# Performance work log

Measured on AMD Instinct MI355X. Metric: run time of the kernel, lower is better.

The kernel has to match this reference:

```python
import jax, jax.numpy as jnp
import numpy as np

B, N, NODE, EDIM, LAT, ENC = 4, 512, 3, 1, 32, 32
NEG = -jnp.inf


def _xavier(key, fan_in, fan_out):
    a = jnp.sqrt(6.0 / (fan_in + fan_out))
    return jax.random.uniform(key, (fan_in, fan_out), jnp.float32, -a, a)


def _mpnn(z, enc_e, adj_b, Wm, Wu):
    """Message: linear([z_i, z_j, e_ij]); adjacency-masked max-aggregation; update linear."""
    zd = z.shape[-1]
    zi = jnp.broadcast_to(z[:, :, None, :], (B, N, N, zd))
    zj = jnp.broadcast_to(z[:, None, :, :], (B, N, N, zd))
    msg = jnp.concatenate([zi, zj, enc_e], axis=-1) @ Wm          # [B,N,N,LAT]
    msg = jnp.where(adj_b[..., None], msg, NEG)
    agg = jnp.max(msg, axis=2)                                    # max over neighbors j
    return jnp.concatenate([z, agg], axis=-1) @ Wu                # [B,N,LAT]


def setup_inputs() -> dict:
    key = jax.random.key(0)
    ks = jax.random.split(key, 16)
    x = jax.random.normal(ks[0], (B, N, NODE), jnp.float32)
    h = jax.random.normal(ks[1], (B, N, LAT), jnp.float32)
    adj = jax.random.randint(ks[2], (B, N, N), 0, 2, jnp.int32)
    e_feat = jax.random.uniform(ks[3], (B, N, N, EDIM), jnp.float32)
    Wn = _xavier(ks[4], LAT + NODE, ENC)          # node_encoder
    We = _xavier(ks[5], EDIM, ENC)                # edge_encoder
    Wm = _xavier(ks[6], 2 * ENC + ENC, LAT)       # processor message
    Wu = _xavier(ks[7], ENC + LAT, LAT)           # processor update
    Wtm = _xavier(ks[8], 2 * LAT + ENC, LAT)      # termination_mpnn message
    Wtu = _xavier(ks[9], LAT + LAT, LAT)          # termination_mpnn update
    Wd = _xavier(ks[10], LAT + ENC, NODE)         # decoder
    Wt = _xavier(ks[11], LAT, 1)                  # termination head
    Wp = _xavier(ks[12], 2 * LAT + ENC, 1)        # predecessor head (pred=1)
    return {"x": x, "h": h, "adj": adj, "e_feat": e_feat, "Wn": Wn, "We": We,
            "Wm": Wm, "Wu": Wu, "Wtm": Wtm, "Wtu": Wtu, "Wd": Wd, "Wt": Wt, "Wp": Wp}


def reference(x, h, adj, e_feat, Wn, We, Wm, Wu, Wtm, Wtu, Wd, Wt, Wp):
    adj2 = adj + jnp.eye(N, dtype=adj.dtype)[None]                # add self-loops
    adj_b = adj2.astype(bool)
    z = jnp.concatenate([x, h], axis=-1) @ Wn                     # [B,N,ENC]
    enc_e = e_feat @ We                                           # [B,N,N,ENC]
    new_h = _mpnn(z, enc_e, adj_b, Wm, Wu) + z                    # [B,N,LAT]
    new_x = jnp.concatenate([z, new_h], axis=-1) @ Wd             # [B,N,NODE]
    tau_node = _mpnn(new_h, enc_e, adj_b, Wtm, Wtu)               # [B,N,LAT]
    tau = jnp.mean(tau_node, axis=1) @ Wt                         # [B,1]
    # predecessor head: all-pairs [h_i, h_j, e_ij] -> scalar, masked by adjacency
    hi = jnp.broadcast_to(new_h[:, :, None, :], (B, N, N, LAT))
    hj = jnp.broadcast_to(new_h[:, None, :, :], (B, N, N, LAT))
    p = (jnp.concatenate([hi, hj, enc_e], axis=-1) @ Wp)[..., 0]  # [B,N,N]
    p = jnp.where(adj_b, p, NEG)
    return new_x, p, tau, new_h
```

## Files before the change

### kernel.cpp

```cpp
#include <hip/hip_runtime.h>

#define XN 512
#define XB 4
#define XSENT (-1.0e30f)
#define XNEG (-3.402823466e38f)

__device__ __forceinline__ float xscrub(float v) {
    unsigned u = __float_as_uint(v);
    u = ((u & 0x7f800000u) == 0x7f800000u) ? 0xff7fffffu : u;
    return __uint_as_float(u);
}

__global__ __launch_bounds__(64) void ne2y_g0(
    const float* __restrict__ We, const float* __restrict__ Wm,
    const float* __restrict__ Wtm, const float* __restrict__ Wtu,
    const float* __restrict__ Wt, const float* __restrict__ Wp,
    float* __restrict__ drv, float* __restrict__ tau_out)
{
    const int t = threadIdx.x;
    if (t < 32) {
        float c1 = 0.f, c2 = 0.f;
        for (int k = 0; k < 32; ++k) {
            const float w = We[k];
            c1 += w * Wm[(64 + k) * 32 + t];
            c2 += w * Wtm[(64 + k) * 32 + t];
        }
        drv[t]      = c1;
        drv[32 + t] = c2;
        float u1 = 0.f, u2 = 0.f;
        for (int k = 0; k < 32; ++k) {
            u1 += Wtu[t * 32 + k]        * Wt[k];
            u2 += Wtu[(32 + t) * 32 + k] * Wt[k];
        }
        drv[64 + t] = u1;
        drv[96 + t] = u2;
        if (t == 0) {
            float cp = 0.f;
            for (int k = 0; k < 32; ++k) cp += We[k] * Wp[64 + k];
            drv[128] = cp;
        }
    }
    if (t < XB) tau_out[t] = 0.f;
}

__global__ __launch_bounds__(256) void ne2y_g1(
    const float* __restrict__ x, const float* __restrict__ h,
    const float* __restrict__ Wn, const float* __restrict__ Wm,
    float* __restrict__ z, float* __restrict__ A1, float* __restrict__ B1)
{
    const int t = threadIdx.x;
    const int r = t >> 5;
    const int l = t & 31;
    const int row = blockIdx.x * 8 + r;
    float acc = 0.f;
    {
        const float* xr = x + row * 3;
        const float* hr = h + row * 32;
        for (int k = 0; k < 3; ++k)  acc += xr[k] * Wn[k * 32 + l];
        for (int k = 0; k < 32; ++k) acc += hr[k] * Wn[(3 + k) * 32 + l];
    }
    __shared__ float zs[8][32];
    zs[r][l] = acc;
    z[row * 32 + l] = acc;
    __syncthreads();
    float a = 0.f, bb = 0.f;
    for (int k = 0; k < 32; ++k) {
        const float zk = zs[r][k];
        a  += zk * Wm[k * 32 + l];
        bb += zk * Wm[(32 + k) * 32 + l];
    }
    A1[row * 32 + l] = a;
    B1[row * 32 + l] = bb;
}

__global__ __launch_bounds__(256) void ne2y_m2(
    const int* __restrict__ adj, const float* __restrict__ ef,
    const float* __restrict__ z, const float* __restrict__ A1,
    const float* __restrict__ B1, const float* __restrict__ drv,
    const float* __restrict__ Wu, const float* __restrict__ Wd,
    const float* __restrict__ Wtm, const float* __restrict__ Wp,
    float* __restrict__ A2, float* __restrict__ B2,
    float* __restrict__ hp1, float* __restrict__ hp2,
    float* __restrict__ o_newx, float* __restrict__ o_newh)
{
    const int q = blockIdx.x;
    const int b = q >> 7;
    const int i0 = (q & 127) * 4;
    const int row0 = b * XN + i0;
    const int t = threadIdx.x;

    __shared__ float ev[4][XN];
    __shared__ int   mk[4][XN];
    {
        const int*   ab = adj + (size_t)row0 * XN;
        const float* eb = ef  + (size_t)row0 * XN;
        for (int u = t; u < 4 * XN; u += 256) {
            const int r = u >> 9, j = u & (XN - 1);
            ev[r][j] = eb[u];
            mk[r][j] = (ab[u] != 0) | (j == i0 + r);
        }
    }
    __syncthreads();

    const int c = t >> 5, l = t & 31;
    const float c1 = drv[l];
    const float* B1b = B1 + (size_t)b * XN * 32;
    float m0 = XNEG, m1 = XNEG, m2v = XNEG, m3v = XNEG;
#pragma unroll 4
    for (int k = 0; k < 64; ++k) {
        const int j = c * 64 + k;
        const float bv = B1b[j * 32 + l];
        float v0 = bv + ev[0][j] * c1;  m0  = fmaxf(m0,  mk[0][j] ? v0 : XNEG);
        float v1 = bv + ev[1][j] * c1;  m1  = fmaxf(m1,  mk[1][j] ? v1 : XNEG);
        float v2 = bv + ev[2][j] * c1;  m2v = fmaxf(m2v, mk[2][j] ? v2 : XNEG);
        float v3 = bv + ev[3][j] * c1;  m3v = fmaxf(m3v, mk[3][j] ? v3 : XNEG);
    }
    __shared__ float red[4][8][33];
    red[0][c][l] = m0;  red[1][c][l] = m1;
    red[2][c][l] = m2v; red[3][c][l] = m3v;
    __syncthreads();

    __shared__ float zs[4][32], ag[4][32], nh[4][32];
    if (t < 128) {
        const int r = t >> 5, ll = t & 31;
        float mm = red[r][0][ll];
        for (int cc = 1; cc < 8; ++cc) mm = fmaxf(mm, red[r][cc][ll]);
        ag[r][ll] = A1[(row0 + r) * 32 + ll] + mm;
        zs[r][ll] = z[(row0 + r) * 32 + ll];
    }
    __syncthreads();
    if (t < 128) {
        const int r = t >> 5, ll = t & 31;
        float v = zs[r][ll];
        for (int k = 0; k < 32; ++k)
            v += zs[r][k] * Wu[k * 32 + ll] + ag[r][k] * Wu[(32 + k) * 32 + ll];
        nh[r][ll] = v;
        o_newh[(row0 + r) * 32 + ll] = v;
    }
    __syncthreads();
    if (t < 128) {
        const int r = t >> 5, ll = t & 31;
        float a2 = 0.f, b2 = 0.f;
        for (int k = 0; k < 32; ++k) {
            const float nk = nh[r][k];
            a2 += nk * Wtm[k * 32 + ll];
            b2 += nk * Wtm[(32 + k) * 32 + ll];
        }
        A2[(row0 + r) * 32 + ll] = a2;
        B2[(row0 + r) * 32 + ll] = b2;
    } else if (t < 136) {
        const int r = (t - 128) >> 1, which = (t - 128) & 1;
        float p = 0.f;
        for (int k = 0; k < 32; ++k) p += nh[r][k] * Wp[which * 32 + k];
        (which ? hp2 : hp1)[row0 + r] = p;
    } else if (t >= 160 && t < 172) {
        const int r = (t - 160) / 3, d = (t - 160) % 3;
        float v = 0.f;
        for (int k = 0; k < 32; ++k)
            v += zs[r][k] * Wd[k * 3 + d] + nh[r][k] * Wd[(32 + k) * 3 + d];
        o_newx[(row0 + r) * 3 + d] = v;
    }
}

__global__ __launch_bounds__(256) void ne2y_m3(
    const int* __restrict__ adj, const float* __restrict__ ef,
    const float* __restrict__ A2, const float* __restrict__ B2,
    const float* __restrict__ newh, const float* __restrict__ hp1,
    const float* __restrict__ hp2, const float* __restrict__ drv,
    float* __restrict__ o_p, float* __restrict__ tau_out)
{
    const int q = blockIdx.x;
    const int b = q >> 7;
    const int i0 = (q & 127) * 4;
    const int row0 = b * XN + i0;
    const int t = threadIdx.x;

    __shared__ float ev[4][XN];
    __shared__ int   mk[4][XN];
    {
        const int*   ab = adj + (size_t)row0 * XN;
        const float* eb = ef  + (size_t)row0 * XN;
        for (int u = t; u < 4 * XN; u += 256) {
            const int r = u >> 9, j = u & (XN - 1);
            ev[r][j] = eb[u];
            mk[r][j] = (ab[u] != 0) | (j == i0 + r);
        }
    }
    __syncthreads();

    {
        const float cp = drv[128];
        const float* h2 = hp2 + b * XN;
#pragma unroll
        for (int r = 0; r < 4; ++r) {
            const float h1 = hp1[row0 + r];
            float* pr = o_p + (size_t)(row0 + r) * XN;
            for (int j = t; j < XN; j += 256) {
                const float v = mk[r][j] ? (h1 + h2[j] + ev[r][j] * cp) : XSENT;
                pr[j] = xscrub(v);
            }
        }
    }

    const int c = t >> 5, l = t & 31;
    const float c2 = drv[32 + l];
    const float* B2b = B2 + (size_t)b * XN * 32;
    float m0 = XNEG, m1 = XNEG, m2v = XNEG, m3v = XNEG;
#pragma unroll 4
    for (int k = 0; k < 64; ++k) {
        const int j = c * 64 + k;
        const float bv = B2b[j * 32 + l];
        float v0 = bv + ev[0][j] * c2;  m0  = fmaxf(m0,  mk[0][j] ? v0 : XNEG);
        float v1 = bv + ev[1][j] * c2;  m1  = fmaxf(m1,  mk[1][j] ? v1 : XNEG);
        float v2 = bv + ev[2][j] * c2;  m2v = fmaxf(m2v, mk[2][j] ? v2 : XNEG);
        float v3 = bv + ev[3][j] * c2;  m3v = fmaxf(m3v, mk[3][j] ? v3 : XNEG);
    }
    __shared__ float red[4][8][33];
    red[0][c][l] = m0;  red[1][c][l] = m1;
    red[2][c][l] = m2v; red[3][c][l] = m3v;
    __syncthreads();

    __shared__ float ss[4][32];
    if (t < 128) {
        const int r = t >> 5, ll = t & 31;
        float mm = red[r][0][ll];
        for (int cc = 1; cc < 8; ++cc) mm = fmaxf(mm, red[r][cc][ll]);
        const float agg = A2[(row0 + r) * 32 + ll] + mm;
        ss[r][ll] = newh[(row0 + r) * 32 + ll] * drv[64 + ll] + agg * drv[96 + ll];
    }
    __syncthreads();
    if (t == 0) {
        float s = 0.f;
        for (int r = 0; r < 4; ++r)
            for (int k = 0; k < 32; ++k) s += ss[r][k];
        atomicAdd(&tau_out[b], s * (1.0f / XN));
    }
}

extern "C" void kernel_launch(void* const* d_in, const int* in_sizes, int n_in,
                              void* d_out, int out_size, void* d_ws, size_t ws_size,
                              hipStream_t stream)
{
    const float* x   = (const float*)d_in[0];
    const float* h   = (const float*)d_in[1];
    const int*   adj = (const int*)  d_in[2];
    const float* ef  = (const float*)d_in[3];
    const float* Wn  = (const float*)d_in[4];
    const float* We  = (const float*)d_in[5];
    const float* Wm  = (const float*)d_in[6];
    const float* Wu  = (const float*)d_in[7];
    const float* Wtm = (const float*)d_in[8];
    const float* Wtu = (const float*)d_in[9];
    const float* Wd  = (const float*)d_in[10];
    const float* Wt  = (const float*)d_in[11];
    const float* Wp  = (const float*)d_in[12];

    float* out    = (float*)d_out;
    float* o_newx = out;
    float* o_p    = out + 6144;
    float* o_tau  = out + 6144 + XB * XN * XN;
    float* o_newh = o_tau + XB;

    float* w = (float*)d_ws;
    const int RN = XB * XN * 32;
    float* z   = w;
    float* A1  = w + RN;
    float* B1  = w + 2 * RN;
    float* A2  = w + 3 * RN;
    float* B2  = w + 4 * RN;
    float* hp1 = w + 5 * RN;
    float* hp2 = w + 5 * RN + XB * XN;
    float* drv = w + 5 * RN + 2 * XB * XN;

    hipLaunchKernelGGL(ne2y_g0, dim3(1), dim3(64), 0, stream,
                       We, Wm, Wtm, Wtu, Wt, Wp, drv, o_tau);
    hipLaunchKernelGGL(ne2y_g1, dim3(XB * XN / 8), dim3(256), 0, stream,
                       x, h, Wn, Wm, z, A1, B1);
    hipLaunchKernelGGL(ne2y_m2, dim3(XB * XN / 4), dim3(256), 0, stream,
                       adj, ef, z, A1, B1, drv, Wu, Wd, Wtm, Wp,
                       A2, B2, hp1, hp2, o_newx, o_newh);
    hipLaunchKernelGGL(ne2y_m3, dim3(XB * XN / 4), dim3(256), 0, stream,
                       adj, ef, A2, B2, o_newh, hp1, hp2, drv, o_p, o_tau);
}
```

Measured before the change: 118.0 us.

## Fuse all stages into one cooperative kernel with grid-wide syncs

Replaces the four separate launches (weight precompute, node encoder, first MPNN, second MPNN plus predecessor head) with a single cooperative kernel that uses grid syncs between phases. Each block loads its adjacency and edge-feature rows into shared memory once and reuses them for both message-passing passes, instead of reading them from global memory twice. Per-row intermediates (z, A1, A2, hp1) and derived weight vectors stay in shared memory, so fewer workspace buffers are written and read. In exchange it adds two grid-wide barriers and requires all 512 blocks to be co-resident, and every block now redundantly recomputes the small weight-derived vectors.

After: 283.4 us. 2.4x slower.

```diff
diff --git a/kernel.cpp b/kernel.cpp
--- a/kernel.cpp
+++ b/kernel.cpp
@@ -1,4 +1,7 @@
 #include <hip/hip_runtime.h>
+#include <hip/hip_cooperative_groups.h>
+
+namespace cg = cooperative_groups;
 
 #define XN 512
 #define XB 4
@@ -11,77 +14,17 @@
     return __uint_as_float(u);
 }
 
-__global__ __launch_bounds__(64) void ne2y_g0(
-    const float* __restrict__ We, const float* __restrict__ Wm,
+__global__ __launch_bounds__(256, 2) void ne2z_fused(
+    const float* __restrict__ x, const float* __restrict__ h,
+    const int* __restrict__ adj, const float* __restrict__ ef,
+    const float* __restrict__ Wn, const float* __restrict__ We,
+    const float* __restrict__ Wm, const float* __restrict__ Wu,
     const float* __restrict__ Wtm, const float* __restrict__ Wtu,
-    const float* __restrict__ Wt, const float* __restrict__ Wp,
-    float* __restrict__ drv, float* __restrict__ tau_out)
-{
-    const int t = threadIdx.x;
-    if (t < 32) {
-        float c1 = 0.f, c2 = 0.f;
-        for (int k = 0; k < 32; ++k) {
-            const float w = We[k];
-            c1 += w * Wm[(64 + k) * 32 + t];
-            c2 += w * Wtm[(64 + k) * 32 + t];
-        }
-        drv[t]      = c1;
-        drv[32 + t] = c2;
-        float u1 = 0.f, u2 = 0.f;
-        for (int k = 0; k < 32; ++k) {
-            u1 += Wtu[t * 32 + k]        * Wt[k];
-            u2 += Wtu[(32 + t) * 32 + k] * Wt[k];
-        }
-        drv[64 + t] = u1;
-        drv[96 + t] = u2;
-        if (t == 0) {
-            float cp = 0.f;
-            for (int k = 0; k < 32; ++k) cp += We[k] * Wp[64 + k];
-            drv[128] = cp;
-        }
-    }
-    if (t < XB) tau_out[t] = 0.f;
-}
-
-__global__ __launch_bounds__(256) void ne2y_g1(
-    const float* __restrict__ x, const float* __restrict__ h,
-    const float* __restrict__ Wn, const float* __restrict__ Wm,
-    float* __restrict__ z, float* __restrict__ A1, float* __restrict__ B1)
-{
-    const int t = threadIdx.x;
-    const int r = t >> 5;
-    const int l = t & 31;
-    const int row = blockIdx.x * 8 + r;
-    float acc = 0.f;
-    {
-        const float* xr = x + row * 3;
-        const float* hr = h + row * 32;
-        for (int k = 0; k < 3; ++k)  acc += xr[k] * Wn[k * 32 + l];
-        for (int k = 0; k < 32; ++k) acc += hr[k] * Wn[(3 + k) * 32 + l];
-    }
-    __shared__ float zs[8][32];
-    zs[r][l] = acc;
-    z[row * 32 + l] = acc;
-    __syncthreads();
-    float a = 0.f, bb = 0.f;
-    for (int k = 0; k < 32; ++k) {
-        const float zk = zs[r][k];
-        a  += zk * Wm[k * 32 + l];
-        bb += zk * Wm[(32 + k) * 32 + l];
-    }
-    A1[row * 32 + l] = a;
-    B1[row * 32 + l] = bb;
-}
-
-__global__ __launch_bounds__(256) void ne2y_m2(
-    const int* __restrict__ adj, const float* __restrict__ ef,
-    const float* __restrict__ z, const float* __restrict__ A1,
-    const float* __restrict__ B1, const float* __restrict__ drv,
-    const float* __restrict__ Wu, const float* __restrict__ Wd,
-    const float* __restrict__ Wtm, const float* __restrict__ Wp,
-    float* __restrict__ A2, float* __restrict__ B2,
-    float* __restrict__ hp1, float* __restrict__ hp2,
-    float* __restrict__ o_newx, float* __restrict__ o_newh)
+    const float* __restrict__ Wd, const float* __restrict__ Wt,
+    const float* __restrict__ Wp,
+    float* __restrict__ B1, float* __restrict__ B2, float* __restrict__ hp2,
+    float* __restrict__ o_newx, float* __restrict__ o_p,
+    float* __restrict__ o_tau, float* __restrict__ o_newh)
 {
     const int q = blockIdx.x;
     const int b = q >> 7;
@@ -91,6 +34,13 @@
 
     __shared__ float ev[4][XN];
     __shared__ int   mk[4][XN];
+    __shared__ float c1s[32], c2s[32], u1s[32], u2s[32];
+    __shared__ float cps;
+    __shared__ float zs[4][32], a1s[4][32], ag[4][32], nh[4][32], a2s[4][32];
+    __shared__ float red[4][8][33];
+    __shared__ float hp1s[4];
+    __shared__ float ss[4][32];
+
     {
         const int*   ab = adj + (size_t)row0 * XN;
         const float* eb = ef  + (size_t)row0 * XN;
@@ -100,33 +50,80 @@
             mk[r][j] = (ab[u] != 0) | (j == i0 + r);
         }
     }
-    __syncthreads();
-
-    const int c = t >> 5, l = t & 31;
-    const float c1 = drv[l];
-    const float* B1b = B1 + (size_t)b * XN * 32;
-    float m0 = XNEG, m1 = XNEG, m2v = XNEG, m3v = XNEG;
+
+    if (t < 32) {
+        float c1 = 0.f, c2 = 0.f;
+        for (int k = 0; k < 32; ++k) {
+            const float w = We[k];
+            c1 += w * Wm[(64 + k) * 32 + t];
+            c2 += w * Wtm[(64 + k) * 32 + t];
+        }
+        c1s[t] = c1;
+        c2s[t] = c2;
+        float u1 = 0.f, u2 = 0.f;
+        for (int k = 0; k < 32; ++k) {
+            u1 += Wtu[t * 32 + k]        * Wt[k];
+            u2 += Wtu[(32 + k) * 32 + t == 0 ? (32 + t) * 32 + k : (32 + t) * 32 + k] * Wt[k];
+        }
+        u1s[t] = u1;
+        u2s[t] = u2;
+        if (t == 0) {
+            float cp = 0.f;
+            for (int k = 0; k < 32; ++k) cp += We[k] * Wp[64 + k];
+            cps = cp;
+        }
+    }
+    if (q == 0 && t < XB) o_tau[t] = 0.f;
+
+    if (t < 128) {
+        const int r = t >> 5, l = t & 31;
+        const int row = row0 + r;
+        float acc = 0.f;
+        const float* xr = x + row * 3;
+        const float* hr = h + row * 32;
+        for (int k = 0; k < 3; ++k)  acc += xr[k] * Wn[k * 32 + l];
+        for (int k = 0; k < 32; ++k) acc += hr[k] * Wn[(3 + k) * 32 + l];
+        zs[r][l] = acc;
+    }
+    __syncthreads();
+    if (t < 128) {
+        const int r = t >> 5, l = t & 31;
+        float a = 0.f, bb = 0.f;
+        for (int k = 0; k < 32; ++k) {
+            const float zk = zs[r][k];
+            a  += zk * Wm[k * 32 + l];
+            bb += zk * Wm[(32 + k) * 32 + l];
+        }
+        a1s[r][l] = a;
+        B1[(row0 + r) * 32 + l] = bb;
+    }
+
+    __threadfence();
+    cg::this_grid().sync();
+
+    {
+        const int c = t >> 5, l = t & 31;
+        const float c1 = c1s[l];
+        const float* B1b = B1 + (size_t)b * XN * 32;
+        float m0 = XNEG, m1 = XNEG, m2v = XNEG, m3v = XNEG;
 #pragma unroll 4
-    for (int k = 0; k < 64; ++k) {
-        const int j = c * 64 + k;
-        const float bv = B1b[j * 32 + l];
-        float v0 = bv + ev[0][j] * c1;  m0  = fmaxf(m0,  mk[0][j] ? v0 : XNEG);
-        float v1 = bv + ev[1][j] * c1;  m1  = fmaxf(m1,  mk[1][j] ? v1 : XNEG);
-        float v2 = bv + ev[2][j] * c1;  m2v = fmaxf(m2v, mk[2][j] ? v2 : XNEG);
-        float v3 = bv + ev[3][j] * c1;  m3v = fmaxf(m3v, mk[3][j] ? v3 : XNEG);
-    }
-    __shared__ float red[4][8][33];
-    red[0][c][l] = m0;  red[1][c][l] = m1;
-    red[2][c][l] = m2v; red[3][c][l] = m3v;
-    __syncthreads();
-
-    __shared__ float zs[4][32], ag[4][32], nh[4][32];
+        for (int k = 0; k < 64; ++k) {
+            const int j = c * 64 + k;
+            const float bv = B1b[j * 32 + l];
+            float v0 = bv + ev[0][j] * c1;  m0  = fmaxf(m0,  mk[0][j] ? v0 : XNEG);
+            float v1 = bv + ev[1][j] * c1;  m1  = fmaxf(m1,  mk[1][j] ? v1 : XNEG);
+            float v2 = bv + ev[2][j] * c1;  m2v = fmaxf(m2v, mk[2][j] ? v2 : XNEG);
+            float v3 = bv + ev[3][j] * c1;  m3v = fmaxf(m3v, mk[3][j] ? v3 : XNEG);
+        }
+        red[0][c][l] = m0;  red[1][c][l] = m1;
+        red[2][c][l] = m2v; red[3][c][l] = m3v;
+    }
+    __syncthreads();
     if (t < 128) {
         const int r = t >> 5, ll = t & 31;
         float mm = red[r][0][ll];
         for (int cc = 1; cc < 8; ++cc) mm = fmaxf(mm, red[r][cc][ll]);
-        ag[r][ll] = A1[(row0 + r) * 32 + ll] + mm;
-        zs[r][ll] = z[(row0 + r) * 32 + ll];
+        ag[r][ll] = a1s[r][ll] + mm;
     }
     __syncthreads();
     if (t < 128) {
@@ -146,13 +143,14 @@
             a2 += nk * Wtm[k * 32 + ll];
             b2 += nk * Wtm[(32 + k) * 32 + ll];
         }
-        A2[(row0 + r) * 32 + ll] = a2;
+        a2s[r][ll] = a2;
         B2[(row0 + r) * 32 + ll] = b2;
     } else if (t < 136) {
         const int r = (t - 128) >> 1, which = (t - 128) & 1;
         float p = 0.f;
         for (int k = 0; k < 32; ++k) p += nh[r][k] * Wp[which * 32 + k];
-        (which ? hp2 : hp1)[row0 + r] = p;
+        if (which) hp2[row0 + r] = p;
+        else       hp1s[r] = p;
     } else if (t >= 160 && t < 172) {
         const int r = (t - 160) / 3, d = (t - 160) % 3;
         float v = 0.f;
@@ -160,40 +158,16 @@
             v += zs[r][k] * Wd[k * 3 + d] + nh[r][k] * Wd[(32 + k) * 3 + d];
         o_newx[(row0 + r) * 3 + d] = v;
     }
-}
-
-__global__ __launch_bounds__(256) void ne2y_m3(
-    const int* __restrict__ adj, const float* __restrict__ ef,
-    const float* __restrict__ A2, const float* __restrict__ B2,
-    const float* __restrict__ newh, const float* __restrict__ hp1,
-    const float* __restrict__ hp2, const float* __restrict__ drv,
-    float* __restrict__ o_p, float* __restrict__ tau_out)
-{
-    const int q = blockIdx.x;
-    const int b = q >> 7;
-    const int i0 = (q & 127) * 4;
-    const int row0 = b * XN + i0;
-    const int t = threadIdx.x;
-
-    __shared__ float ev[4][XN];
-    __shared__ int   mk[4][XN];
-    {
-        const int*   ab = adj + (size_t)row0 * XN;
-        const float* eb = ef  + (size_t)row0 * XN;
-        for (int u = t; u < 4 * XN; u += 256) {
-            const int r = u >> 9, j = u & (XN - 1);
-            ev[r][j] = eb[u];
-            mk[r][j] = (ab[u] != 0) | (j == i0 + r);
-        }
-    }
-    __syncthreads();
-
-    {
-        const float cp = drv[128];
+
+    __threadfence();
+    cg::this_grid().sync();
+
+    {
+        const float cp = cps;
         const float* h2 = hp2 + b * XN;
 #pragma unroll
         for (int r = 0; r < 4; ++r) {
-            const float h1 = hp1[row0 + r];
+            const float h1 = hp1s[r];
             float* pr = o_p + (size_t)(row0 + r) * XN;
             for (int j = t; j < XN; j += 256) {
                 const float v = mk[r][j] ? (h1 + h2[j] + ev[r][j] * cp) : XSENT;
@@ -201,39 +175,37 @@
             }
         }
     }
-
-    const int c = t >> 5, l = t & 31;
-    const float c2 = drv[32 + l];
-    const float* B2b = B2 + (size_t)b * XN * 32;
-    float m0 = XNEG, m1 = XNEG, m2v = XNEG, m3v = XNEG;
+    {
+        const int c = t >> 5, l = t & 31;
+        const float c2 = c2s[l];
+        const float* B2b = B2 + (size_t)b * XN * 32;
+        float m0 = XNEG, m1 = XNEG, m2v = XNEG, m3v = XNEG;
 #pragma unroll 4
-    for (int k = 0; k < 64; ++k) {
-        const int j = c * 64 + k;
-        const float bv = B2b[j * 32 + l];
-        float v0 = bv + ev[0][j] * c2;  m0  = fmaxf(m0,  mk[0][j] ? v0 : XNEG);
-        float v1 = bv + ev[1][j] * c2;  m1  = fmaxf(m1,  mk[1][j] ? v1 : XNEG);
-        float v2 = bv + ev[2][j] * c2;  m2v = fmaxf(m2v, mk[2][j] ? v2 : XNEG);
-        float v3 = bv + ev[3][j] * c2;  m3v = fmaxf(m3v, mk[3][j] ? v3 : XNEG);
-    }
-    __shared__ float red[4][8][33];
-    red[0][c][l] = m0;  red[1][c][l] = m1;
-    red[2][c][l] = m2v; red[3][c][l] = m3v;
-    __syncthreads();
-
-    __shared__ float ss[4][32];
+        for (int k = 0; k < 64; ++k) {
+            const int j = c * 64 + k;
+            const float bv = B2b[j * 32 + l];
+            float v0 = bv + ev[0][j] * c2;  m0  = fmaxf(m0,  mk[0][j] ? v0 : XNEG);
+            float v1 = bv + ev[1][j] * c2;  m1  = fmaxf(m1,  mk[1][j] ? v1 : XNEG);
+            float v2 = bv + ev[2][j] * c2;  m2v = fmaxf(m2v, mk[2][j] ? v2 : XNEG);
+            float v3 = bv + ev[3][j] * c2;  m3v = fmaxf(m3v, mk[3][j] ? v3 : XNEG);
+        }
+        red[0][c][l] = m0;  red[1][c][l] = m1;
+        red[2][c][l] = m2v; red[3][c][l] = m3v;
+    }
+    __syncthreads();
     if (t < 128) {
         const int r = t >> 5, ll = t & 31;
         float mm = red[r][0][ll];
         for (int cc = 1; cc < 8; ++cc) mm = fmaxf(mm, red[r][cc][ll]);
-        const float agg = A2[(row0 + r) * 32 + ll] + mm;
-        ss[r][ll] = newh[(row0 + r) * 32 + ll] * drv[64 + ll] + agg * drv[96 + ll];
+        const float agg = a2s[r][ll] + mm;
+        ss[r][ll] = nh[r][ll] * u1s[ll] + agg * u2s[ll];
     }
     __syncthreads();
     if (t == 0) {
         float s = 0.f;
         for (int r = 0; r < 4; ++r)
             for (int k = 0; k < 32; ++k) s += ss[r][k];
-        atomicAdd(&tau_out[b], s * (1.0f / XN));
+        atomicAdd(&o_tau[b], s * (1.0f / XN));
     }
 }
 
@@ -263,22 +235,17 @@
 
     float* w = (float*)d_ws;
     const int RN = XB * XN * 32;
-    float* z   = w;
-    float* A1  = w + RN;
-    float* B1  = w + 2 * RN;
-    float* A2  = w + 3 * RN;
-    float* B2  = w + 4 * RN;
-    float* hp1 = w + 5 * RN;
-    float* hp2 = w + 5 * RN + XB * XN;
-    float* drv = w + 5 * RN + 2 * XB * XN;
-
-    hipLaunchKernelGGL(ne2y_g0, dim3(1), dim3(64), 0, stream,
-                       We, Wm, Wtm, Wtu, Wt, Wp, drv, o_tau);
-    hipLaunchKernelGGL(ne2y_g1, dim3(XB * XN / 8), dim3(256), 0, stream,
-                       x, h, Wn, Wm, z, A1, B1);
-    hipLaunchKernelGGL(ne2y_m2, dim3(XB * XN / 4), dim3(256), 0, stream,
-                       adj, ef, z, A1, B1, drv, Wu, Wd, Wtm, Wp,
-                       A2, B2, hp1, hp2, o_newx, o_newh);
-    hipLaunchKernelGGL(ne2y_m3, dim3(XB * XN / 4), dim3(256), 0, stream,
-                       adj, ef, A2, B2, o_newh, hp1, hp2, drv, o_p, o_tau);
+    float* B1  = w;
+    float* B2  = w + RN;
+    float* hp2 = w + 2 * RN;
+
+    void* args[] = {
+        (void*)&x, (void*)&h, (void*)&adj, (void*)&ef,
+        (void*)&Wn, (void*)&We, (void*)&Wm, (void*)&Wu,
+        (void*)&Wtm, (void*)&Wtu, (void*)&Wd, (void*)&Wt, (void*)&Wp,
+        (void*)&B1, (void*)&B2, (void*)&hp2,
+        (void*)&o_newx, (void*)&o_p, (void*)&o_tau, (void*)&o_newh
+    };
+    hipLaunchCooperativeKernel((const void*)ne2z_fused,
+                               dim3(XB * XN / 4), dim3(256), args, 0, stream);
 }
```

## Fold adjacency mask into NaN-tagged edge values, merge setup kernel, vectorize loads

Applied to the files above, without the earlier changes.

The adjacency mask is now encoded directly into the shared edge-value array as quiet NaNs, which fmaxf ignores. This removes the separate int mask array and the per-element selects in the max loops. Adjacency and edge features are loaded as int4/float4, the weight-derivation kernel is merged into the first GEMV kernel to drop one launch, and the tau reduction uses a wavefront shuffle instead of a serial loop. Correctness now depends on fmaxf returning the non-NaN operand and on the predecessor output mapping NaN/Inf to the sentinel.

Measured after the change: 111.3 us. 1.06x faster.

```diff
diff --git a/kernel.cpp b/kernel.cpp
--- a/kernel.cpp
+++ b/kernel.cpp
@@ -4,51 +4,44 @@
 #define XB 4
 #define XSENT (-1.0e30f)
 #define XNEG (-3.402823466e38f)
-
-__device__ __forceinline__ float xscrub(float v) {
-    unsigned u = __float_as_uint(v);
-    u = ((u & 0x7f800000u) == 0x7f800000u) ? 0xff7fffffu : u;
-    return __uint_as_float(u);
-}
-
-__global__ __launch_bounds__(64) void ne2y_g0(
-    const float* __restrict__ We, const float* __restrict__ Wm,
-    const float* __restrict__ Wtm, const float* __restrict__ Wtu,
-    const float* __restrict__ Wt, const float* __restrict__ Wp,
-    float* __restrict__ drv, float* __restrict__ tau_out)
-{
-    const int t = threadIdx.x;
-    if (t < 32) {
-        float c1 = 0.f, c2 = 0.f;
-        for (int k = 0; k < 32; ++k) {
-            const float w = We[k];
-            c1 += w * Wm[(64 + k) * 32 + t];
-            c2 += w * Wtm[(64 + k) * 32 + t];
-        }
-        drv[t]      = c1;
-        drv[32 + t] = c2;
-        float u1 = 0.f, u2 = 0.f;
-        for (int k = 0; k < 32; ++k) {
-            u1 += Wtu[t * 32 + k]        * Wt[k];
-            u2 += Wtu[(32 + t) * 32 + k] * Wt[k];
-        }
-        drv[64 + t] = u1;
-        drv[96 + t] = u2;
-        if (t == 0) {
-            float cp = 0.f;
-            for (int k = 0; k < 32; ++k) cp += We[k] * Wp[64 + k];
-            drv[128] = cp;
-        }
-    }
-    if (t < XB) tau_out[t] = 0.f;
-}
-
-__global__ __launch_bounds__(256) void ne2y_g1(
+#define QNANU 0x7fc00000u
+
+__global__ __launch_bounds__(256) void ne2r_g1(
     const float* __restrict__ x, const float* __restrict__ h,
     const float* __restrict__ Wn, const float* __restrict__ Wm,
-    float* __restrict__ z, float* __restrict__ A1, float* __restrict__ B1)
+    const float* __restrict__ We, const float* __restrict__ Wtm,
+    const float* __restrict__ Wtu, const float* __restrict__ Wt,
+    const float* __restrict__ Wp,
+    float* __restrict__ z, float* __restrict__ A1, float* __restrict__ B1,
+    float* __restrict__ drv, float* __restrict__ tau_out)
 {
     const int t = threadIdx.x;
+    if (blockIdx.x == 0) {
+        if (t < 32) {
+            float c1 = 0.f, c2 = 0.f;
+            for (int k = 0; k < 32; ++k) {
+                const float w = We[k];
+                c1 += w * Wm[(64 + k) * 32 + t];
+                c2 += w * Wtm[(64 + k) * 32 + t];
+            }
+            drv[t]      = c1;
+            drv[32 + t] = c2;
+            float u1 = 0.f, u2 = 0.f;
+            for (int k = 0; k < 32; ++k) {
+                u1 += Wtu[t * 32 + k]        * Wt[k];
+                u2 += Wtu[(32 + t) * 32 + k] * Wt[k];
+            }
+            drv[64 + t] = u1;
+            drv[96 + t] = u2;
+            if (t == 0) {
+                float cp = 0.f;
+                for (int k = 0; k < 32; ++k) cp += We[k] * Wp[64 + k];
+                drv[128] = cp;
+            }
+        } else if (t >= 64 && t < 64 + XB) {
+            tau_out[t - 64] = 0.f;
+        }
+    }
     const int r = t >> 5;
     const int l = t & 31;
     const int row = blockIdx.x * 8 + r;
@@ -73,7 +66,7 @@
     B1[row * 32 + l] = bb;
 }
 
-__global__ __launch_bounds__(256) void ne2y_m2(
+__global__ __launch_bounds__(256) void ne2r_m2(
     const int* __restrict__ adj, const float* __restrict__ ef,
     const float* __restrict__ z, const float* __restrict__ A1,
     const float* __restrict__ B1, const float* __restrict__ drv,
@@ -88,16 +81,22 @@
     const int i0 = (q & 127) * 4;
     const int row0 = b * XN + i0;
     const int t = threadIdx.x;
+    const float qnan = __uint_as_float(QNANU);
 
     __shared__ float ev[4][XN];
-    __shared__ int   mk[4][XN];
-    {
-        const int*   ab = adj + (size_t)row0 * XN;
-        const float* eb = ef  + (size_t)row0 * XN;
-        for (int u = t; u < 4 * XN; u += 256) {
-            const int r = u >> 9, j = u & (XN - 1);
-            ev[r][j] = eb[u];
-            mk[r][j] = (ab[u] != 0) | (j == i0 + r);
+    {
+        const int4*   ab4 = (const int4*)  (adj + (size_t)row0 * XN);
+        const float4* eb4 = (const float4*)(ef  + (size_t)row0 * XN);
+        for (int u = t; u < XN; u += 256) {
+            const int4   a4 = ab4[u];
+            const float4 e4 = eb4[u];
+            const int r  = u >> 7;
+            const int j0 = (u & 127) << 2;
+            const int self = i0 + r;
+            ev[r][j0 + 0] = (a4.x || (j0 + 0) == self) ? e4.x : qnan;
+            ev[r][j0 + 1] = (a4.y || (j0 + 1) == self) ? e4.y : qnan;
+            ev[r][j0 + 2] = (a4.z || (j0 + 2) == self) ? e4.z : qnan;
+            ev[r][j0 + 3] = (a4.w || (j0 + 3) == self) ? e4.w : qnan;
         }
     }
     __syncthreads();
@@ -110,10 +109,10 @@
     for (int k = 0; k < 64; ++k) {
         const int j = c * 64 + k;
         const float bv = B1b[j * 32 + l];
-        float v0 = bv + ev[0][j] * c1;  m0  = fmaxf(m0,  mk[0][j] ? v0 : XNEG);
-        float v1 = bv + ev[1][j] * c1;  m1  = fmaxf(m1,  mk[1][j] ? v1 : XNEG);
-        float v2 = bv + ev[2][j] * c1;  m2v = fmaxf(m2v, mk[2][j] ? v2 : XNEG);
-        float v3 = bv + ev[3][j] * c1;  m3v = fmaxf(m3v, mk[3][j] ? v3 : XNEG);
+        m0  = fmaxf(m0,  fmaf(ev[0][j], c1, bv));
+        m1  = fmaxf(m1,  fmaf(ev[1][j], c1, bv));
+        m2v = fmaxf(m2v, fmaf(ev[2][j], c1, bv));
+        m3v = fmaxf(m3v, fmaf(ev[3][j], c1, bv));
     }
     __shared__ float red[4][8][33];
     red[0][c][l] = m0;  red[1][c][l] = m1;
@@ -162,7 +161,7 @@
     }
 }
 
-__global__ __launch_bounds__(256) void ne2y_m3(
+__global__ __launch_bounds__(256) void ne2r_m3(
     const int* __restrict__ adj, const float* __restrict__ ef,
     const float* __restrict__ A2, const float* __restrict__ B2,
     const float* __restrict__ newh, const float* __restrict__ hp1,
@@ -174,16 +173,22 @@
     const int i0 = (q & 127) * 4;
     const int row0 = b * XN + i0;
     const int t = threadIdx.x;
+    const float qnan = __uint_as_float(QNANU);
 
     __shared__ float ev[4][XN];
-    __shared__ int   mk[4][XN];
-    {
-        const int*   ab = adj + (size_t)row0 * XN;
-        const float* eb = ef  + (size_t)row0 * XN;
-        for (int u = t; u < 4 * XN; u += 256) {
-            const int r = u >> 9, j = u & (XN - 1);
-            ev[r][j] = eb[u];
-            mk[r][j] = (ab[u] != 0) | (j == i0 + r);
+    {
+        const int4*   ab4 = (const int4*)  (adj + (size_t)row0 * XN);
+        const float4* eb4 = (const float4*)(ef  + (size_t)row0 * XN);
+        for (int u = t; u < XN; u += 256) {
+            const int4   a4 = ab4[u];
+            const float4 e4 = eb4[u];
+            const int r  = u >> 7;
+            const int j0 = (u & 127) << 2;
+            const int self = i0 + r;
+            ev[r][j0 + 0] = (a4.x || (j0 + 0) == self) ? e4.x : qnan;
+            ev[r][j0 + 1] = (a4.y || (j0 + 1) == self) ? e4.y : qnan;
+            ev[r][j0 + 2] = (a4.z || (j0 + 2) == self) ? e4.z : qnan;
+            ev[r][j0 + 3] = (a4.w || (j0 + 3) == self) ? e4.w : qnan;
         }
     }
     __syncthreads();
@@ -196,8 +201,9 @@
             const float h1 = hp1[row0 + r];
             float* pr = o_p + (size_t)(row0 + r) * XN;
             for (int j = t; j < XN; j += 256) {
-                const float v = mk[r][j] ? (h1 + h2[j] + ev[r][j] * cp) : XSENT;
-                pr[j] = xscrub(v);
+                const float pv = fmaf(ev[r][j], cp, h1 + h2[j]);
+                const unsigned bv = __float_as_uint(pv);
+                pr[j] = ((bv & 0x7f800000u) == 0x7f800000u) ? XSENT : pv;
             }
         }
     }
@@ -210,10 +216,10 @@
     for (int k = 0; k < 64; ++k) {
         const int j = c * 64 + k;
         const float bv = B2b[j * 32 + l];
-        float v0 = bv + ev[0][j] * c2;  m0  = fmaxf(m0,  mk[0][j] ? v0 : XNEG);
-        float v1 = bv + ev[1][j] * c2;  m1  = fmaxf(m1,  mk[1][j] ? v1 : XNEG);
-        float v2 = bv + ev[2][j] * c2;  m2v = fmaxf(m2v, mk[2][j] ? v2 : XNEG);
-        float v3 = bv + ev[3][j] * c2;  m3v = fmaxf(m3v, mk[3][j] ? v3 : XNEG);
+        m0  = fmaxf(m0,  fmaf(ev[0][j], c2, bv));
+        m1  = fmaxf(m1,  fmaf(ev[1][j], c2, bv));
+        m2v = fmaxf(m2v, fmaf(ev[2][j], c2, bv));
+        m3v = fmaxf(m3v, fmaf(ev[3][j], c2, bv));
     }
     __shared__ float red[4][8][33];
     red[0][c][l] = m0;  red[1][c][l] = m1;
@@ -229,11 +235,12 @@
         ss[r][ll] = newh[(row0 + r) * 32 + ll] * drv[64 + ll] + agg * drv[96 + ll];
     }
     __syncthreads();
-    if (t == 0) {
-        float s = 0.f;
-        for (int r = 0; r < 4; ++r)
-            for (int k = 0; k < 32; ++k) s += ss[r][k];
-        atomicAdd(&tau_out[b], s * (1.0f / XN));
+    if (t < 64) {
+        const float* ssf = &ss[0][0];
+        float s = ssf[t] + ssf[t + 64];
+#pragma unroll
+        for (int o = 32; o > 0; o >>= 1) s += __shfl_down(s, o);
+        if (t == 0) atomicAdd(&tau_out[b], s * (1.0f / XN));
     }
 }
 
@@ -272,13 +279,11 @@
     float* hp2 = w + 5 * RN + XB * XN;
     float* drv = w + 5 * RN + 2 * XB * XN;
 
-    hipLaunchKernelGGL(ne2y_g0, dim3(1), dim3(64), 0, stream,
-                       We, Wm, Wtm, Wtu, Wt, Wp, drv, o_tau);
-    hipLaunchKernelGGL(ne2y_g1, dim3(XB * XN / 8), dim3(256), 0, stream,
-                       x, h, Wn, Wm, z, A1, B1);
-    hipLaunchKernelGGL(ne2y_m2, dim3(XB * XN / 4), dim3(256), 0, stream,
+    hipLaunchKernelGGL(ne2r_g1, dim3(XB * XN / 8), dim3(256), 0, stream,
+                       x, h, Wn, Wm, We, Wtm, Wtu, Wt, Wp, z, A1, B1, drv, o_tau);
+    hipLaunchKernelGGL(ne2r_m2, dim3(XB * XN / 4), dim3(256), 0, stream,
                        adj, ef, z, A1, B1, drv, Wu, Wd, Wtm, Wp,
                        A2, B2, hp1, hp2, o_newx, o_newh);
-    hipLaunchKernelGGL(ne2y_m3, dim3(XB * XN / 4), dim3(256), 0, stream,
+    hipLaunchKernelGGL(ne2r_m3, dim3(XB * XN / 4), dim3(256), 0, stream,
                        adj, ef, A2, B2, o_newh, hp1, hp2, drv, o_p, o_tau);
 }
```
